# Kernel tuning notes

Measured on AMD Instinct MI355X. Metric: run time of the kernel, lower is better.

The kernel has to match this reference:

```python
import jax, jax.numpy as jnp
import numpy as np

DIM, HEADS = 128, 8
DH = DIM // HEADS
SCALE = DH ** -0.5
N, E = 50000, 800000


def setup_inputs() -> dict:
    key = jax.random.key(0)
    ks = jax.random.split(key, 12)
    w = lambda k: jax.random.normal(k, (DIM, DIM), dtype=jnp.float32) * 0.02
    b = lambda k: jax.random.normal(k, (DIM,), dtype=jnp.float32) * 0.02
    return {
        "q_nodes": jax.random.normal(ks[0], (N, DIM), dtype=jnp.float32),
        "k_edges": jax.random.normal(ks[1], (E, DIM), dtype=jnp.float32),
        "v_edges": jax.random.normal(ks[2], (E, DIM), dtype=jnp.float32),
        "edge_index": jax.random.randint(ks[3], (2, E), 0, N, dtype=jnp.int64),
        "Wq": w(ks[4]), "bq": b(ks[5]),
        "Wk": w(ks[6]), "bk": b(ks[7]),
        "Wv": w(ks[8]), "bv": b(ks[9]),
        "Wo": w(ks[10]), "bo": b(ks[11]),
    }


def reference(q_nodes, k_edges, v_edges, edge_index, Wq, bq, Wk, bk, Wv, bv, Wo, bo):
    n, e = q_nodes.shape[0], k_edges.shape[0]
    dst = edge_index[0]  # src (edge_index[1]) is unused by the module
    q = (q_nodes @ Wq.T + bq).reshape(n, HEADS, DH)
    k = (k_edges @ Wk.T + bk).reshape(e, HEADS, DH)
    v = (v_edges @ Wv.T + bv).reshape(e, HEADS, DH)
    # per-edge score: dot(q[dst], k) per head -> [E, H]
    score = jnp.einsum('ehd,ehd->eh', q[dst], k) * SCALE
    # segment (per-dst-node) softmax over edges, numerically stable
    m = jax.ops.segment_max(score, dst, num_segments=n)          # [N, H]
    ex = jnp.exp(score - m[dst])                                  # [E, H]
    s = jax.ops.segment_sum(ex, dst, num_segments=n)             # [N, H]
    w = ex / (s[dst] + 1e-16)                                     # [E, H]
    weighted_v = (v * w[..., None]).reshape(e, DIM)               # [E, dim]
    aggr = jax.ops.segment_sum(weighted_v, dst, num_segments=n)  # [N, dim]
    return aggr @ Wo.T + bo
```

## Files before the change

### kernel.cpp

```cpp
#include <hip/hip_runtime.h>

#define TM 64
#define NTHREADS 256
#define PAD 132

typedef __attribute__((ext_vector_type(8))) short short8;
typedef __attribute__((ext_vector_type(4))) float f32x4;

__device__ __forceinline__ short f2bf(float f) {
  union { float f; unsigned u; } uf; uf.f = f;
  unsigned r = uf.u + 0x7FFFu + ((uf.u >> 16) & 1u);
  return (short)(r >> 16);
}
__device__ __forceinline__ float bf2f(short s) {
  union { unsigned u; float f; } uf; uf.u = ((unsigned)(unsigned short)s) << 16;
  return uf.f;
}
__device__ __forceinline__ short8 pack8(float4 a, float4 b) {
  short8 r;
  r[0] = f2bf(a.x); r[1] = f2bf(a.y); r[2] = f2bf(a.z); r[3] = f2bf(a.w);
  r[4] = f2bf(b.x); r[5] = f2bf(b.y); r[6] = f2bf(b.z); r[7] = f2bf(b.w);
  return r;
}


__global__ __launch_bounds__(512) void proj_mfma(
    const float* __restrict__ X, const short* __restrict__ Wb,
    const float* __restrict__ bias, float* __restrict__ Y, int M, float scale) {
  __shared__ short Xb[8192];
  int t = threadIdx.x;
  int w = t >> 6, l = t & 63, g = l >> 4, c = l & 15;
  short8 wf[4];
#pragma unroll
  for (int kc = 0; kc < 4; ++kc)
    wf[kc] = *(const short8*)(Wb + (w * 16 + c) * 128 + kc * 32 + g * 8);
  float4 b4 = *(const float4*)(bias + w * 16 + g * 4);

  for (int rb = blockIdx.x * 64; rb < M; rb += gridDim.x * 64) {
    {
      int r = t >> 3, q8 = t & 7;
      int row = rb + r; if (row >= M) row = M - 1;
      const float4* xs = (const float4*)(X + (size_t)row * 128 + q8 * 16);
      float4 x0 = xs[0], x1 = xs[1], x2 = xs[2], x3 = xs[3];
      int sw = (r & 7) << 4;
      *(short8*)((char*)Xb + r * 256 + ((q8 * 32) ^ sw)) = pack8(x0, x1);
      *(short8*)((char*)Xb + r * 256 + ((q8 * 32 + 16) ^ sw)) = pack8(x2, x3);
    }
    __syncthreads();
#pragma unroll
    for (int et = 0; et < 4; ++et) {
      int rl = et * 16 + c;
      f32x4 acc = {};
      int sw = (rl & 7) << 4;
#pragma unroll
      for (int kc = 0; kc < 4; ++kc) {
        short8 xb = *(const short8*)((char*)Xb + rl * 256 + ((kc * 64 + g * 16) ^ sw));
        acc = __builtin_amdgcn_mfma_f32_16x16x32_bf16(wf[kc], xb, acc, 0, 0, 0);
      }
      int row = rb + rl;
      if (row < M) {
        float4 o;
        o.x = (acc[0] + b4.x) * scale; o.y = (acc[1] + b4.y) * scale;
        o.z = (acc[2] + b4.z) * scale; o.w = (acc[3] + b4.w) * scale;
        *(float4*)(Y + (size_t)row * 128 + w * 16 + g * 4) = o;
      }
    }
    __syncthreads();
  }
}


__global__ __launch_bounds__(256) void hist_kernel(const int* __restrict__ dst,
                                                   int* __restrict__ cnt, int E) {
  int e = blockIdx.x * 256 + threadIdx.x;
  if (e < E) atomicAdd(&cnt[dst[e]], 1);
}

__global__ __launch_bounds__(1024) void scan_part(const int* __restrict__ cnt,
                                                  int* __restrict__ part, int N) {
  __shared__ int ws[16];
  int t = threadIdx.x, i = blockIdx.x * 1024 + t;
  int v = (i < N) ? cnt[i] : 0;
#pragma unroll
  for (int d = 1; d < 64; d <<= 1) v += __shfl_xor(v, d);
  if ((t & 63) == 0) ws[t >> 6] = v;
  __syncthreads();
  if (t < 16) {
    int x = ws[t];
#pragma unroll
    for (int d = 1; d < 16; d <<= 1) x += __shfl_xor(x, d);
    if (t == 0) part[blockIdx.x] = x;
  }
}

__global__ __launch_bounds__(64) void scan_offs(int* __restrict__ part, int P) {
  int t = threadIdx.x;
  int carry = 0;
  for (int base = 0; base < P; base += 64) {
    int i = base + t;
    int v = (i < P) ? part[i] : 0;
    int x = v;
#pragma unroll
    for (int d = 1; d < 64; d <<= 1) { int y = __shfl_up(x, d); if (t >= d) x += y; }
    if (i < P) part[i] = x - v + carry;
    carry += __shfl(x, 63);
  }
}

__global__ __launch_bounds__(1024) void scan_final(const int* __restrict__ cnt,
                                                   const int* __restrict__ part,
                                                   int* __restrict__ rp,
                                                   int* __restrict__ cur, int N) {
  __shared__ int ws[16];
  __shared__ int wofs[16];
  int t = threadIdx.x, i = blockIdx.x * 1024 + t;
  int lane = t & 63, wid = t >> 6;
  int v = (i < N) ? cnt[i] : 0;
  int x = v;
#pragma unroll
  for (int d = 1; d < 64; d <<= 1) { int y = __shfl_up(x, d); if (lane >= d) x += y; }
  if (lane == 63) ws[wid] = x;
  __syncthreads();
  if (t == 0) {
    int s = 0;
#pragma unroll
    for (int k2 = 0; k2 < 16; ++k2) { int tmp = ws[k2]; wofs[k2] = s; s += tmp; }
  }
  __syncthreads();
  int incl = x + wofs[wid] + part[blockIdx.x];
  int excl = incl - v;
  if (i < N) {
    rp[i] = excl; cur[i] = excl;
    if (i == N - 1) rp[N] = incl;
  }
}

__global__ __launch_bounds__(256) void perm_kernel(const int* __restrict__ dst,
                                                   int* __restrict__ cursor,
                                                   int* __restrict__ perm, int E) {
  int e = blockIdx.x * 256 + threadIdx.x;
  if (e < E) perm[e] = atomicAdd(&cursor[dst[e]], 1);
}

__global__ __launch_bounds__(256) void wprep4(
    const float* __restrict__ Wq, const float* __restrict__ Wk,
    const float* __restrict__ Wv, const float* __restrict__ Wo,
    short* __restrict__ wqb, short* __restrict__ wkb,
    short* __restrict__ wvb, short* __restrict__ wob) {
  int i = blockIdx.x * 256 + threadIdx.x;
  if (i < 16384) {
    wqb[i] = f2bf(Wq[i]); wkb[i] = f2bf(Wk[i]);
    wvb[i] = f2bf(Wv[i]); wob[i] = f2bf(Wo[i]);
  }
}


__global__ __launch_bounds__(512) void edge_mfma4(
    const float* __restrict__ K, const float* __restrict__ V,
    const int* __restrict__ eidx, const int* __restrict__ perm,
    const short* __restrict__ wkb, const short* __restrict__ wvb,
    const float* __restrict__ bk, const float* __restrict__ qp,
    float* __restrict__ exb, short* __restrict__ wv, int E) {
  __shared__ short Kb[8192];
  __shared__ short Vb[8192];
  __shared__ float exs[512];
  __shared__ int sh_perm[64];
  int t = threadIdx.x;
  int w = t >> 6, l = t & 63, g = l >> 4, c = l & 15;
  short8 wK[4], wV[4];
#pragma unroll
  for (int kc = 0; kc < 4; ++kc) {
    wK[kc] = *(const short8*)(wkb + (w * 16 + c) * 128 + kc * 32 + g * 8);
    wV[kc] = *(const short8*)(wvb + (w * 16 + c) * 128 + kc * 32 + g * 8);
  }
  float4 bk4 = *(const float4*)(bk + w * 16 + g * 4);

  int r = t >> 3, q8 = t & 7;
  int sw_st = (r & 7) << 4;
  int b0 = r * 256 + ((q8 * 32) ^ sw_st);
  int stride = gridDim.x * 64;
  int eb = blockIdx.x * 64;

  float4 k0, k1, k2, k3;
  float4 qv[4];
  int prm_r;
  {
    int row0 = eb + r; if (row0 >= E) row0 = E - 1;
    const float4* ks = (const float4*)(K + (size_t)row0 * 128 + q8 * 16);
    k0 = ks[0]; k1 = ks[1]; k2 = ks[2]; k3 = ks[3];
    prm_r = perm[row0];
    int d0[4];
#pragma unroll
    for (int et = 0; et < 4; ++et) {
      int e = eb + et * 16 + c; if (e >= E) e = E - 1;
      d0[et] = eidx[e];
    }
#pragma unroll
    for (int et = 0; et < 4; ++et)
      qv[et] = *(const float4*)(qp + (size_t)d0[et] * 128 + w * 16 + g * 4);
  }

  for (; eb < E; eb += stride) {
    int ebn = eb + stride;
    bool hn = ebn < E;

    __syncthreads();
    *(short8*)((char*)Kb + b0) = pack8(k0, k1);
    *(short8*)((char*)Kb + (b0 ^ 16)) = pack8(k2, k3);
    if (q8 == 0) sh_perm[r] = prm_r;
    float4 v0, v1, v2, v3;
    {
      int rowv = eb + r; if (rowv >= E) rowv = E - 1;
      const float4* vs = (const float4*)(V + (size_t)rowv * 128 + q8 * 16);
      v0 = vs[0]; v1 = vs[1]; v2 = vs[2]; v3 = vs[3];
    }
    int dn[4], prm_rn = 0;
    if (hn) {
      int rowk = ebn + r; if (rowk >= E) rowk = E - 1;
      prm_rn = perm[rowk];
#pragma unroll
      for (int et = 0; et < 4; ++et) {
        int e = ebn + et * 16 + c; if (e >= E) e = E - 1;
        dn[et] = eidx[e];
      }
    }
    __syncthreads();

    float ex[4];
#pragma unroll
    for (int et = 0; et < 4; ++et) {
      int eloc = et * 16 + c;
      int swr = (eloc & 7) << 4;
      f32x4 acc = {};
#pragma unroll
      for (int kc = 0; kc < 4; ++kc) {
        short8 xb = *(const short8*)((char*)Kb + eloc * 256 + ((kc * 64 + g * 16) ^ swr));
        acc = __builtin_amdgcn_mfma_f32_16x16x32_bf16(wK[kc], xb, acc, 0, 0, 0);
      }
      float s = (acc[0] + bk4.x) * qv[et].x + (acc[1] + bk4.y) * qv[et].y +
                (acc[2] + bk4.z) * qv[et].z + (acc[3] + bk4.w) * qv[et].w;
      s += __shfl_xor(s, 16);
      s += __shfl_xor(s, 32);
      ex[et] = __expf(s);
      if (g == 0) exs[eloc * 8 + w] = ex[et];
    }

    *(short8*)((char*)Vb + b0) = pack8(v0, v1);
    *(short8*)((char*)Vb + (b0 ^ 16)) = pack8(v2, v3);
    if (hn) {
      int rowk = ebn + r; if (rowk >= E) rowk = E - 1;
      const float4* ks = (const float4*)(K + (size_t)rowk * 128 + q8 * 16);
      k0 = ks[0]; k1 = ks[1]; k2 = ks[2]; k3 = ks[3];
#pragma unroll
      for (int et = 0; et < 4; ++et)
        qv[et] = *(const float4*)(qp + (size_t)dn[et] * 128 + w * 16 + g * 4);
    }
    __syncthreads();

#pragma unroll
    for (int et = 0; et < 4; ++et) {
      int eloc = et * 16 + c;
      int swr = (eloc & 7) << 4;
      f32x4 acc = {};
#pragma unroll
      for (int kc = 0; kc < 4; ++kc) {
        short8 xb = *(const short8*)((char*)Vb + eloc * 256 + ((kc * 64 + g * 16) ^ swr));
        acc = __builtin_amdgcn_mfma_f32_16x16x32_bf16(wV[kc], xb, acc, 0, 0, 0);
      }
      short4 sv;
      sv.x = f2bf(acc[0] * ex[et]); sv.y = f2bf(acc[1] * ex[et]);
      sv.z = f2bf(acc[2] * ex[et]); sv.w = f2bf(acc[3] * ex[et]);
      *(short4*)((char*)Kb + eloc * 256 + ((w * 32 + g * 8) ^ swr)) = sv;
    }
    __syncthreads();

    {
      int row = eb + r;
      if (row < E) {
        int slot = sh_perm[r];
        short8 a = *(const short8*)((char*)Kb + r * 256 + ((q8 * 32) ^ sw_st));
        short8 b = *(const short8*)((char*)Kb + r * 256 + ((q8 * 32 + 16) ^ sw_st));
        *(short8*)(wv + (size_t)slot * 128 + q8 * 16) = a;
        *(short8*)(wv + (size_t)slot * 128 + q8 * 16 + 8) = b;
      }
      if (t < 128) {
        int r2 = t >> 1, half = t & 1;
        if (eb + r2 < E) {
          int slot2 = sh_perm[r2];
          *(float4*)(exb + (size_t)slot2 * 8 + half * 4) =
              *(const float4*)(&exs[r2 * 8 + half * 4]);
        }
      }
    }
    prm_r = prm_rn;
  }
}


__global__ __launch_bounds__(256) void pull3(
    const short* __restrict__ wv, const float* __restrict__ exb,
    const int* __restrict__ rp, const float* __restrict__ bv,
    float* __restrict__ aggr, int N) {
  int w = threadIdx.x >> 6, l = threadIdx.x & 63;
  int n = blockIdx.x * 4 + w;
  if (n >= N) return;
  int beg = rp[n], end = rp[n + 1];
  int h = l >> 3;
  float a0 = 0.f, a1 = 0.f, s = 0.f;
  int j = beg;
  for (; j + 1 < end; j += 2) {
    unsigned u0 = *(const unsigned*)(wv + (size_t)j * 128 + l * 2);
    unsigned u1 = *(const unsigned*)(wv + (size_t)(j + 1) * 128 + l * 2);
    float s0 = exb[(size_t)j * 8 + h], s1 = exb[(size_t)(j + 1) * 8 + h];
    a0 += bf2f((short)(u0 & 0xFFFFu)) + bf2f((short)(u1 & 0xFFFFu));
    a1 += bf2f((short)(u0 >> 16)) + bf2f((short)(u1 >> 16));
    s += s0 + s1;
  }
  if (j < end) {
    unsigned u0 = *(const unsigned*)(wv + (size_t)j * 128 + l * 2);
    s += exb[(size_t)j * 8 + h];
    a0 += bf2f((short)(u0 & 0xFFFFu));
    a1 += bf2f((short)(u0 >> 16));
  }
  float2 o;
  if (end > beg) {
    float inv = 1.f / (s + 1e-16f);
    float2 bvv = *(const float2*)(bv + l * 2);
    o.x = a0 * inv + bvv.x; o.y = a1 * inv + bvv.y;
  } else {
    o.x = 0.f; o.y = 0.f;
  }
  *(float2*)(aggr + (size_t)n * 128 + l * 2) = o;
}


__device__ __forceinline__ void stage_x(float (*Xs)[PAD], const float* __restrict__ X,
                                        int rowbase, int M, int t) {
#pragma unroll
  for (int i = 0; i < 8; ++i) {
    int idx = t + NTHREADS * i;
    int r = idx >> 5, q = idx & 31;
    int row = rowbase + r;
    if (row >= M) row = M - 1;
    const float4 v = *(const float4*)(X + (size_t)row * 128 + q * 4);
    *(float4*)(&Xs[r][q * 4]) = v;
  }
}

__device__ __forceinline__ void gemm_tile(const float (*Xs)[PAD], float (*WT)[PAD],
                                          const float* __restrict__ W,
                                          float acc[8][4], int r0, int c0, int t) {
#pragma unroll 1
  for (int kk = 0; kk < 128; kk += 32) {
    {
      int j = t >> 1, half = t & 1;
      const float* src = W + j * 128 + kk + half * 16;
      float4 a = *(const float4*)(src);
      float4 b = *(const float4*)(src + 4);
      float4 c = *(const float4*)(src + 8);
      float4 d = *(const float4*)(src + 12);
      int cb = half * 16;
      WT[cb + 0][j] = a.x;  WT[cb + 1][j] = a.y;  WT[cb + 2][j] = a.z;  WT[cb + 3][j] = a.w;
      WT[cb + 4][j] = b.x;  WT[cb + 5][j] = b.y;  WT[cb + 6][j] = b.z;  WT[cb + 7][j] = b.w;
      WT[cb + 8][j] = c.x;  WT[cb + 9][j] = c.y;  WT[cb + 10][j] = c.z; WT[cb + 11][j] = c.w;
      WT[cb + 12][j] = d.x; WT[cb + 13][j] = d.y; WT[cb + 14][j] = d.z; WT[cb + 15][j] = d.w;
    }
    __syncthreads();
#pragma unroll
    for (int c2 = 0; c2 < 16; ++c2) {
      float4 wa = *(const float4*)(&WT[2 * c2][c0]);
      float4 wb = *(const float4*)(&WT[2 * c2 + 1][c0]);
#pragma unroll
      for (int i = 0; i < 8; ++i) {
        float2 xv = *(const float2*)(&Xs[r0 + i][kk + 2 * c2]);
        acc[i][0] = fmaf(xv.x, wa.x, acc[i][0]);
        acc[i][1] = fmaf(xv.x, wa.y, acc[i][1]);
        acc[i][2] = fmaf(xv.x, wa.z, acc[i][2]);
        acc[i][3] = fmaf(xv.x, wa.w, acc[i][3]);
        acc[i][0] = fmaf(xv.y, wb.x, acc[i][0]);
        acc[i][1] = fmaf(xv.y, wb.y, acc[i][1]);
        acc[i][2] = fmaf(xv.y, wb.z, acc[i][2]);
        acc[i][3] = fmaf(xv.y, wb.w, acc[i][3]);
      }
    }
    __syncthreads();
  }
}

__global__ __launch_bounds__(NTHREADS) void proj_kernel(
    const float* __restrict__ X, const float* __restrict__ W,
    const float* __restrict__ b, float* __restrict__ Y, int M) {
  __shared__ float Xs[TM][PAD];
  __shared__ float WT[32][PAD];
  int t = threadIdx.x;
  int B0 = blockIdx.x * TM;
  stage_x(Xs, X, B0, M, t);
  __syncthreads();
  int r0 = (t >> 5) * 8, m = t & 31, c0 = m * 4;
  float acc[8][4] = {};
  gemm_tile(Xs, WT, W, acc, r0, c0, t);
  float4 bv = ((const float4*)b)[m];
#pragma unroll
  for (int i = 0; i < 8; ++i) {
    int row = B0 + r0 + i;
    if (row < M) {
      float4 o;
      o.x = acc[i][0] + bv.x; o.y = acc[i][1] + bv.y;
      o.z = acc[i][2] + bv.z; o.w = acc[i][3] + bv.w;
      *(float4*)(Y + (size_t)row * 128 + c0) = o;
    }
  }
}

__global__ __launch_bounds__(NTHREADS) void edge_kernel(
    const float* __restrict__ Kin, const float* __restrict__ Vin,
    const int* __restrict__ eidx,
    const float* __restrict__ Wk, const float* __restrict__ bk,
    const float* __restrict__ Wv, const float* __restrict__ bv,
    const float* __restrict__ qp, float* __restrict__ s_sum,
    float* __restrict__ aggr, int E) {
  __shared__ float Xs[TM][PAD];
  __shared__ float WT[32][PAD];
  __shared__ int dsts[TM];
  int t = threadIdx.x;
  int e0 = blockIdx.x * TM;
  if (t < TM) {
    int idx = e0 + t;
    if (idx >= E) idx = E - 1;
    dsts[t] = eidx[idx];
  }
  stage_x(Xs, Kin, e0, E, t);
  __syncthreads();
  int r0 = (t >> 5) * 8, m = t & 31, c0 = m * 4;
  int h = m >> 2;
  float acc[8][4] = {};
  gemm_tile(Xs, WT, Wk, acc, r0, c0, t);
  float4 bkv = ((const float4*)bk)[m];
  float ex[8];
#pragma unroll
  for (int i = 0; i < 8; ++i) {
    int r = r0 + i;
    const float4 qv = *(const float4*)(qp + (size_t)dsts[r] * 128 + c0);
    float p = (acc[i][0] + bkv.x) * qv.x + (acc[i][1] + bkv.y) * qv.y +
              (acc[i][2] + bkv.z) * qv.z + (acc[i][3] + bkv.w) * qv.w;
    p += __shfl_xor(p, 1);
    p += __shfl_xor(p, 2);
    float e = __expf(p * 0.25f);
    ex[i] = e;
    if ((m & 3) == 0 && (e0 + r) < E)
      atomicAdd(&s_sum[(size_t)dsts[r] * 8 + h], e);
  }
  __syncthreads();
  stage_x(Xs, Vin, e0, E, t);
  __syncthreads();
#pragma unroll
  for (int i = 0; i < 8; ++i)
#pragma unroll
    for (int j = 0; j < 4; ++j) acc[i][j] = 0.f;
  gemm_tile(Xs, WT, Wv, acc, r0, c0, t);
  float4 bvv = ((const float4*)bv)[m];
#pragma unroll
  for (int i = 0; i < 8; ++i) {
    int r = r0 + i;
    if ((e0 + r) < E) {
      size_t base = (size_t)dsts[r] * 128 + c0;
      atomicAdd(&aggr[base + 0], (acc[i][0] + bvv.x) * ex[i]);
      atomicAdd(&aggr[base + 1], (acc[i][1] + bvv.y) * ex[i]);
      atomicAdd(&aggr[base + 2], (acc[i][2] + bvv.z) * ex[i]);
      atomicAdd(&aggr[base + 3], (acc[i][3] + bvv.w) * ex[i]);
    }
  }
}

__global__ __launch_bounds__(NTHREADS) void out_kernel(
    const float* __restrict__ aggr, const float* __restrict__ s_sum,
    const float* __restrict__ W, const float* __restrict__ b,
    float* __restrict__ Y, int M) {
  __shared__ float Xs[TM][PAD];
  __shared__ float WT[32][PAD];
  int t = threadIdx.x;
  int B0 = blockIdx.x * TM;
#pragma unroll
  for (int i = 0; i < 8; ++i) {
    int idx = t + NTHREADS * i;
    int r = idx >> 5, q = idx & 31;
    int row = B0 + r;
    if (row >= M) row = M - 1;
    float4 v = *(const float4*)(aggr + (size_t)row * 128 + q * 4);
    float inv = 1.0f / (s_sum[(size_t)row * 8 + (q >> 2)] + 1e-16f);
    v.x *= inv; v.y *= inv; v.z *= inv; v.w *= inv;
    *(float4*)(&Xs[r][q * 4]) = v;
  }
  __syncthreads();
  int r0 = (t >> 5) * 8, m = t & 31, c0 = m * 4;
  float acc[8][4] = {};
  gemm_tile(Xs, WT, W, acc, r0, c0, t);
  float4 bv = ((const float4*)b)[m];
#pragma unroll
  for (int i = 0; i < 8; ++i) {
    int row = B0 + r0 + i;
    if (row < M) {
      float4 o;
      o.x = acc[i][0] + bv.x; o.y = acc[i][1] + bv.y;
      o.z = acc[i][2] + bv.z; o.w = acc[i][3] + bv.w;
      *(float4*)(Y + (size_t)row * 128 + c0) = o;
    }
  }
}


extern "C" void kernel_launch(void* const* d_in, const int* in_sizes, int n_in,
                              void* d_out, int out_size, void* d_ws, size_t ws_size,
                              hipStream_t stream) {
  const float* q_nodes = (const float*)d_in[0];
  const float* k_edges = (const float*)d_in[1];
  const float* v_edges = (const float*)d_in[2];
  const int* eidx = (const int*)d_in[3];
  const float* Wq = (const float*)d_in[4];
  const float* bq = (const float*)d_in[5];
  const float* Wk = (const float*)d_in[6];
  const float* bk = (const float*)d_in[7];
  const float* Wv = (const float*)d_in[8];
  const float* bv = (const float*)d_in[9];
  const float* Wo = (const float*)d_in[10];
  const float* bo = (const float*)d_in[11];

  int N = in_sizes[0] / 128;
  int E = in_sizes[1] / 128;
  int P = (N + 1023) / 1024;

  size_t off = 0;
  auto alloc = [&](size_t b) { size_t o = off; off += (b + 255) & ~(size_t)255; return o; };
  size_t o_qp   = alloc((size_t)N * 128 * 4);
  size_t o_aggr = alloc((size_t)N * 128 * 4);
  size_t o_exb  = alloc((size_t)E * 8 * 4);
  size_t o_rp   = alloc(((size_t)N + 1) * 4);
  size_t o_cur  = alloc((size_t)N * 4);
  size_t o_cnt  = alloc((size_t)N * 4);
  size_t o_perm = alloc((size_t)E * 4);
  size_t o_part = alloc((size_t)(P + 1) * 4);
  size_t o_wqb  = alloc((size_t)16384 * 2);
  size_t o_wkb  = alloc((size_t)16384 * 2);
  size_t o_wvb  = alloc((size_t)16384 * 2);
  size_t o_wob  = alloc((size_t)16384 * 2);
  size_t o_wv   = alloc((size_t)E * 128 * 2);

  if (off <= ws_size) {
    char* base = (char*)d_ws;
    float* qp    = (float*)(base + o_qp);
    float* aggr  = (float*)(base + o_aggr);
    float* exb   = (float*)(base + o_exb);
    int*   rp    = (int*)(base + o_rp);
    int*   cur   = (int*)(base + o_cur);
    int*   cnt   = (int*)(base + o_cnt);
    int*   perm  = (int*)(base + o_perm);
    int*   part  = (int*)(base + o_part);
    short* wqb   = (short*)(base + o_wqb);
    short* wkb   = (short*)(base + o_wkb);
    short* wvb   = (short*)(base + o_wvb);
    short* wob   = (short*)(base + o_wob);
    short* wvbuf = (short*)(base + o_wv);

    hipMemsetAsync(cnt, 0, (size_t)N * 4, stream);
    wprep4<<<64, 256, 0, stream>>>(Wq, Wk, Wv, Wo, wqb, wkb, wvb, wob);
    proj_mfma<<<(N + 63) / 64, 512, 0, stream>>>(q_nodes, wqb, bq, qp, N, 0.25f);
    hist_kernel<<<(E + 255) / 256, 256, 0, stream>>>(eidx, cnt, E);
    scan_part<<<P, 1024, 0, stream>>>(cnt, part, N);
    scan_offs<<<1, 64, 0, stream>>>(part, P);
    scan_final<<<P, 1024, 0, stream>>>(cnt, part, rp, cur, N);
    perm_kernel<<<(E + 255) / 256, 256, 0, stream>>>(eidx, cur, perm, E);

    int eblk = (E + 63) / 64; if (eblk > 1024) eblk = 1024;
    edge_mfma4<<<eblk, 512, 0, stream>>>(k_edges, v_edges, eidx, perm, wkb, wvb,
                                         bk, qp, exb, wvbuf, E);
    pull3<<<(N + 3) / 4, 256, 0, stream>>>(wvbuf, exb, rp, bv, aggr, N);
    proj_mfma<<<(N + 63) / 64, 512, 0, stream>>>(aggr, wob, bo, (float*)d_out, N, 1.0f);
  } else {
    float* q_proj = (float*)d_ws;
    float* s_sum  = q_proj + (size_t)N * 128;
    float* aggr   = s_sum + (size_t)N * 8;
    hipMemsetAsync(s_sum, 0, (size_t)N * 136 * sizeof(float), stream);
    int nblk = (N + TM - 1) / TM;
    int eblk = (E + TM - 1) / TM;
    proj_kernel<<<nblk, NTHREADS, 0, stream>>>(q_nodes, Wq, bq, q_proj, N);
    edge_kernel<<<eblk, NTHREADS, 0, stream>>>(k_edges, v_edges, eidx, Wk, bk, Wv, bv,
                                               q_proj, s_sum, aggr, E);
    out_kernel<<<nblk, NTHREADS, 0, stream>>>(aggr, s_sum, Wo, bo, (float*)d_out, N);
  }
}
```

Baseline: 428.8 us.

## Fuse segment pull with output projection and restage q gathers in edge kernel

The per-node pull (softmax-normalized aggregation) is merged with the output projection into one kernel. Each block gathers 64 node rows, packs them to bf16 in LDS and runs the MFMA projection, so the fp32 aggr buffer no longer goes to and from global memory and one launch disappears. The edge kernel now fetches dst indices and q rows for the current tile inside the loop, interleaved with the K-phase MFMAs, instead of prefetching them for the next tile. This frees registers but may expose gather latency. The fused kernel runs with fewer waves per node, which can lower memory parallelism in the pull.

```diff
diff --git a/kernel.cpp b/kernel.cpp
--- a/kernel.cpp
+++ b/kernel.cpp
@@ -155,7 +155,7 @@
 }
 
 
-__global__ __launch_bounds__(512) void edge_mfma4(
+__global__ __launch_bounds__(512) void edge_mfma5(
     const float* __restrict__ K, const float* __restrict__ V,
     const int* __restrict__ eidx, const int* __restrict__ perm,
     const short* __restrict__ wkb, const short* __restrict__ wvb,
@@ -182,22 +182,12 @@
   int eb = blockIdx.x * 64;
 
   float4 k0, k1, k2, k3;
-  float4 qv[4];
   int prm_r;
   {
     int row0 = eb + r; if (row0 >= E) row0 = E - 1;
     const float4* ks = (const float4*)(K + (size_t)row0 * 128 + q8 * 16);
     k0 = ks[0]; k1 = ks[1]; k2 = ks[2]; k3 = ks[3];
     prm_r = perm[row0];
-    int d0[4];
-#pragma unroll
-    for (int et = 0; et < 4; ++et) {
-      int e = eb + et * 16 + c; if (e >= E) e = E - 1;
-      d0[et] = eidx[e];
-    }
-#pragma unroll
-    for (int et = 0; et < 4; ++et)
-      qv[et] = *(const float4*)(qp + (size_t)d0[et] * 128 + w * 16 + g * 4);
   }
 
   for (; eb < E; eb += stride) {
@@ -214,36 +204,43 @@
       const float4* vs = (const float4*)(V + (size_t)rowv * 128 + q8 * 16);
       v0 = vs[0]; v1 = vs[1]; v2 = vs[2]; v3 = vs[3];
     }
-    int dn[4], prm_rn = 0;
-    if (hn) {
-      int rowk = ebn + r; if (rowk >= E) rowk = E - 1;
-      prm_rn = perm[rowk];
-#pragma unroll
-      for (int et = 0; et < 4; ++et) {
-        int e = ebn + et * 16 + c; if (e >= E) e = E - 1;
-        dn[et] = eidx[e];
-      }
+    int d[4];
+#pragma unroll
+    for (int et = 0; et < 4; ++et) {
+      int e = eb + et * 16 + c; if (e >= E) e = E - 1;
+      d[et] = eidx[e];
     }
     __syncthreads();
 
     float ex[4];
-#pragma unroll
-    for (int et = 0; et < 4; ++et) {
-      int eloc = et * 16 + c;
-      int swr = (eloc & 7) << 4;
-      f32x4 acc = {};
-#pragma unroll
-      for (int kc = 0; kc < 4; ++kc) {
-        short8 xb = *(const short8*)((char*)Kb + eloc * 256 + ((kc * 64 + g * 16) ^ swr));
-        acc = __builtin_amdgcn_mfma_f32_16x16x32_bf16(wK[kc], xb, acc, 0, 0, 0);
-      }
-      float s = (acc[0] + bk4.x) * qv[et].x + (acc[1] + bk4.y) * qv[et].y +
-                (acc[2] + bk4.z) * qv[et].z + (acc[3] + bk4.w) * qv[et].w;
-      s += __shfl_xor(s, 16);
-      s += __shfl_xor(s, 32);
-      ex[et] = __expf(s);
-      if (g == 0) exs[eloc * 8 + w] = ex[et];
-    }
+    const float* qpb = qp + (size_t)(w * 16 + g * 4);
+    float4 qv0 = *(const float4*)(qpb + (size_t)d[0] * 128);
+    float4 qv1 = *(const float4*)(qpb + (size_t)d[1] * 128);
+#define KPHASE_ET(ET, QV)                                                          \
+    {                                                                              \
+      int eloc = (ET) * 16 + c;                                                    \
+      int swr = (eloc & 7) << 4;                                                   \
+      f32x4 acc = {};                                                              \
+      _Pragma("unroll")                                                            \
+      for (int kc = 0; kc < 4; ++kc) {                                             \
+        short8 xb = *(const short8*)((char*)Kb + eloc * 256 +                      \
+                                     ((kc * 64 + g * 16) ^ swr));                  \
+        acc = __builtin_amdgcn_mfma_f32_16x16x32_bf16(wK[kc], xb, acc, 0, 0, 0);   \
+      }                                                                            \
+      float s = (acc[0] + bk4.x) * (QV).x + (acc[1] + bk4.y) * (QV).y +            \
+                (acc[2] + bk4.z) * (QV).z + (acc[3] + bk4.w) * (QV).w;             \
+      s += __shfl_xor(s, 16);                                                      \
+      s += __shfl_xor(s, 32);                                                      \
+      ex[ET] = __expf(s);                                                          \
+      if (g == 0) exs[eloc * 8 + w] = ex[ET];                                      \
+    }
+    KPHASE_ET(0, qv0)
+    float4 qv2 = *(const float4*)(qpb + (size_t)d[2] * 128);
+    KPHASE_ET(1, qv1)
+    float4 qv3 = *(const float4*)(qpb + (size_t)d[3] * 128);
+    KPHASE_ET(2, qv2)
+    KPHASE_ET(3, qv3)
+#undef KPHASE_ET
 
     *(short8*)((char*)Vb + b0) = pack8(v0, v1);
     *(short8*)((char*)Vb + (b0 ^ 16)) = pack8(v2, v3);
@@ -251,9 +248,7 @@
       int rowk = ebn + r; if (rowk >= E) rowk = E - 1;
       const float4* ks = (const float4*)(K + (size_t)rowk * 128 + q8 * 16);
       k0 = ks[0]; k1 = ks[1]; k2 = ks[2]; k3 = ks[3];
-#pragma unroll
-      for (int et = 0; et < 4; ++et)
-        qv[et] = *(const float4*)(qp + (size_t)dn[et] * 128 + w * 16 + g * 4);
+      prm_r = perm[rowk];
     }
     __syncthreads();
 
@@ -292,45 +287,86 @@
         }
       }
     }
-    prm_r = prm_rn;
-  }
-}
-
-
-__global__ __launch_bounds__(256) void pull3(
+  }
+}
+
+
+__global__ __launch_bounds__(512) void proj_out_pull(
     const short* __restrict__ wv, const float* __restrict__ exb,
-    const int* __restrict__ rp, const float* __restrict__ bv,
-    float* __restrict__ aggr, int N) {
-  int w = threadIdx.x >> 6, l = threadIdx.x & 63;
-  int n = blockIdx.x * 4 + w;
-  if (n >= N) return;
-  int beg = rp[n], end = rp[n + 1];
+    const int* __restrict__ rp, const float* __restrict__ bvv,
+    const short* __restrict__ Wb, const float* __restrict__ bias,
+    float* __restrict__ Y, int N) {
+  __shared__ short Xb[8192];
+  int t = threadIdx.x;
+  int w = t >> 6, l = t & 63, g = l >> 4, c = l & 15;
+  short8 wf[4];
+#pragma unroll
+  for (int kc = 0; kc < 4; ++kc)
+    wf[kc] = *(const short8*)(Wb + (w * 16 + c) * 128 + kc * 32 + g * 8);
+  float4 b4 = *(const float4*)(bias + w * 16 + g * 4);
+  float2 bv2 = *(const float2*)(bvv + l * 2);
   int h = l >> 3;
-  float a0 = 0.f, a1 = 0.f, s = 0.f;
-  int j = beg;
-  for (; j + 1 < end; j += 2) {
-    unsigned u0 = *(const unsigned*)(wv + (size_t)j * 128 + l * 2);
-    unsigned u1 = *(const unsigned*)(wv + (size_t)(j + 1) * 128 + l * 2);
-    float s0 = exb[(size_t)j * 8 + h], s1 = exb[(size_t)(j + 1) * 8 + h];
-    a0 += bf2f((short)(u0 & 0xFFFFu)) + bf2f((short)(u1 & 0xFFFFu));
-    a1 += bf2f((short)(u0 >> 16)) + bf2f((short)(u1 >> 16));
-    s += s0 + s1;
-  }
-  if (j < end) {
-    unsigned u0 = *(const unsigned*)(wv + (size_t)j * 128 + l * 2);
-    s += exb[(size_t)j * 8 + h];
-    a0 += bf2f((short)(u0 & 0xFFFFu));
-    a1 += bf2f((short)(u0 >> 16));
-  }
-  float2 o;
-  if (end > beg) {
-    float inv = 1.f / (s + 1e-16f);
-    float2 bvv = *(const float2*)(bv + l * 2);
-    o.x = a0 * inv + bvv.x; o.y = a1 * inv + bvv.y;
-  } else {
-    o.x = 0.f; o.y = 0.f;
-  }
-  *(float2*)(aggr + (size_t)n * 128 + l * 2) = o;
+
+  for (int rb = blockIdx.x * 64; rb < N; rb += gridDim.x * 64) {
+#pragma unroll 1
+    for (int i = 0; i < 8; ++i) {
+      int rl = w * 8 + i;
+      int n = rb + rl;
+      float a0 = 0.f, a1 = 0.f, s = 0.f;
+      bool nonempty = false;
+      if (n < N) {
+        int beg = rp[n], end = rp[n + 1];
+        nonempty = end > beg;
+        int j = beg;
+        for (; j + 1 < end; j += 2) {
+          unsigned u0 = *(const unsigned*)(wv + (size_t)j * 128 + l * 2);
+          unsigned u1 = *(const unsigned*)(wv + (size_t)(j + 1) * 128 + l * 2);
+          float s0 = exb[(size_t)j * 8 + h], s1 = exb[(size_t)(j + 1) * 8 + h];
+          a0 += bf2f((short)(u0 & 0xFFFFu)) + bf2f((short)(u1 & 0xFFFFu));
+          a1 += bf2f((short)(u0 >> 16)) + bf2f((short)(u1 >> 16));
+          s += s0 + s1;
+        }
+        if (j < end) {
+          unsigned u0 = *(const unsigned*)(wv + (size_t)j * 128 + l * 2);
+          s += exb[(size_t)j * 8 + h];
+          a0 += bf2f((short)(u0 & 0xFFFFu));
+          a1 += bf2f((short)(u0 >> 16));
+        }
+      }
+      float x0, x1;
+      if (nonempty) {
+        float inv = 1.f / (s + 1e-16f);
+        x0 = a0 * inv + bv2.x; x1 = a1 * inv + bv2.y;
+      } else {
+        x0 = 0.f; x1 = 0.f;
+      }
+      unsigned packed = ((unsigned)(unsigned short)f2bf(x1) << 16) |
+                        (unsigned short)f2bf(x0);
+      int sw = (rl & 7) << 4;
+      *(unsigned*)((char*)Xb + rl * 256 + ((l * 4) ^ sw)) = packed;
+    }
+    __syncthreads();
+
+#pragma unroll
+    for (int et = 0; et < 4; ++et) {
+      int rl = et * 16 + c;
+      f32x4 acc = {};
+      int sw = (rl & 7) << 4;
+#pragma unroll
+      for (int kc = 0; kc < 4; ++kc) {
+        short8 xb = *(const short8*)((char*)Xb + rl * 256 + ((kc * 64 + g * 16) ^ sw));
+        acc = __builtin_amdgcn_mfma_f32_16x16x32_bf16(wf[kc], xb, acc, 0, 0, 0);
+      }
+      int row = rb + rl;
+      if (row < N) {
+        float4 o;
+        o.x = acc[0] + b4.x; o.y = acc[1] + b4.y;
+        o.z = acc[2] + b4.z; o.w = acc[3] + b4.w;
+        *(float4*)(Y + (size_t)row * 128 + w * 16 + g * 4) = o;
+      }
+    }
+    __syncthreads();
+  }
 }
 
 
@@ -532,7 +568,6 @@
   size_t off = 0;
   auto alloc = [&](size_t b) { size_t o = off; off += (b + 255) & ~(size_t)255; return o; };
   size_t o_qp   = alloc((size_t)N * 128 * 4);
-  size_t o_aggr = alloc((size_t)N * 128 * 4);
   size_t o_exb  = alloc((size_t)E * 8 * 4);
   size_t o_rp   = alloc(((size_t)N + 1) * 4);
   size_t o_cur  = alloc((size_t)N * 4);
@@ -548,7 +583,6 @@
   if (off <= ws_size) {
     char* base = (char*)d_ws;
     float* qp    = (float*)(base + o_qp);
-    float* aggr  = (float*)(base + o_aggr);
     float* exb   = (float*)(base + o_exb);
     int*   rp    = (int*)(base + o_rp);
     int*   cur   = (int*)(base + o_cur);
@@ -571,10 +605,10 @@
     perm_kernel<<<(E + 255) / 256, 256, 0, stream>>>(eidx, cur, perm, E);
 
     int eblk = (E + 63) / 64; if (eblk > 1024) eblk = 1024;
-    edge_mfma4<<<eblk, 512, 0, stream>>>(k_edges, v_edges, eidx, perm, wkb, wvb,
+    edge_mfma5<<<eblk, 512, 0, stream>>>(k_edges, v_edges, eidx, perm, wkb, wvb,
                                          bk, qp, exb, wvbuf, E);
-    pull3<<<(N + 3) / 4, 256, 0, stream>>>(wvbuf, exb, rp, bv, aggr, N);
-    proj_mfma<<<(N + 63) / 64, 512, 0, stream>>>(aggr, wob, bo, (float*)d_out, N, 1.0f);
+    proj_out_pull<<<(N + 63) / 64, 512, 0, stream>>>(wvbuf, exb, rp, bv, wob, bo,
+                                                     (float*)d_out, N);
   } else {
     float* q_proj = (float*)d_ws;
     float* s_sum  = q_proj + (size_t)N * 128;
```

New measurement: 466.0 us. 8.7% more time.
